# Kernel tuning notes

Measured on AMD Instinct MI355X. Metric: run time of the kernel, lower is better.

Reference implementation:

```python
import jax, jax.numpy as jnp
import numpy as np

D_IN = 1024
D_OUT = 1024
NUM_HEAD = 16
HEAD_DIM = D_OUT // NUM_HEAD


def setup_inputs() -> dict:
    key = jax.random.key(0)
    ks = jax.random.split(key, 7)
    B, S = 2, 2048
    X = jax.random.normal(ks[0], (B, S, D_IN), dtype=jnp.float32)
    scale = 1.0 / np.sqrt(D_IN)
    Wq = jax.random.normal(ks[1], (D_IN, D_OUT), dtype=jnp.float32) * scale
    Wk = jax.random.normal(ks[2], (D_IN, D_OUT), dtype=jnp.float32) * scale
    Wv = jax.random.normal(ks[3], (D_IN, D_OUT), dtype=jnp.float32) * scale
    bq = jax.random.normal(ks[4], (D_OUT,), dtype=jnp.float32) * 0.01
    bk = jax.random.normal(ks[5], (D_OUT,), dtype=jnp.float32) * 0.01
    bv = jax.random.normal(ks[6], (D_OUT,), dtype=jnp.float32) * 0.01
    return {"X": X, "Wq": Wq, "bq": bq, "Wk": Wk, "bk": bk, "Wv": Wv, "bv": bv}


def reference(X, Wq, bq, Wk, bk, Wv, bv):
    B, S, _ = X.shape
    # QKV projections, reshape to [B, H, S, Dh]
    def proj(W, b):
        y = jnp.einsum('bsi,io->bso', X, W) + b
        return y.reshape(B, S, NUM_HEAD, HEAD_DIM).transpose(0, 2, 1, 3)
    Q = proj(Wq, bq)
    K = proj(Wk, bk)
    V = proj(Wv, bv)
    # NOTE: original divides by head_dim**2 (not sqrt(head_dim)) -- kept faithful.
    scores = jnp.einsum('bhqd,bhkd->bhqk', Q, K) / (HEAD_DIM ** 2)
    attn = jax.nn.softmax(scores, axis=-1)  # dropout is identity at eval
    out = jnp.einsum('bhqk,bhkd->bhqd', attn, V)
    return out.transpose(0, 2, 1, 3).reshape(B, S, D_OUT)
```

## Files before the change

### kernel.cpp

```cpp
#include <hip/hip_runtime.h>
#include <hip/hip_bf16.h>

typedef __attribute__((ext_vector_type(8))) short frag8;
typedef __attribute__((ext_vector_type(8))) unsigned short u16x8;
typedef __attribute__((ext_vector_type(4))) float f32x4;

__device__ __forceinline__ unsigned short f2b(float x) {
    unsigned int u = __float_as_uint(x);
    return (unsigned short)((u + 0x7FFFu + ((u >> 16) & 1u)) >> 16);
}

__device__ __forceinline__ int swz(int row, int scol) {
    return (row << 6) + (scol ^ ((row & 7) << 3));
}

__global__ __launch_bounds__(256) void xcvt_kernel(const float* __restrict__ X,
                                                   unsigned short* __restrict__ Xb)
{
    const int i = (blockIdx.x * 256 + threadIdx.x) * 8;
    float4 a = *reinterpret_cast<const float4*>(X + i);
    float4 b = *reinterpret_cast<const float4*>(X + i + 4);
    u16x8 v;
    v[0] = f2b(a.x); v[1] = f2b(a.y); v[2] = f2b(a.z); v[3] = f2b(a.w);
    v[4] = f2b(b.x); v[5] = f2b(b.y); v[6] = f2b(b.z); v[7] = f2b(b.w);
    *reinterpret_cast<u16x8*>(Xb + i) = v;
}

__global__ __launch_bounds__(256) void transpose_w_kernel(
    const float* __restrict__ Wq, const float* __restrict__ Wk, const float* __restrict__ Wv,
    unsigned short* __restrict__ Wtq, unsigned short* __restrict__ Wtk, unsigned short* __restrict__ Wtv)
{
    const float* W = blockIdx.z == 0 ? Wq : (blockIdx.z == 1 ? Wk : Wv);
    unsigned short* Wt = blockIdx.z == 0 ? Wtq : (blockIdx.z == 1 ? Wtk : Wtv);
    __shared__ unsigned short tile[64 * 72];
    const int t = threadIdx.x;
    const int k0 = blockIdx.x * 64, n0 = blockIdx.y * 64;
#pragma unroll
    for (int r = 0; r < 16; ++r) {
        int k = r * 4 + (t >> 6), n = t & 63;
        tile[n * 72 + k] = f2b(W[(size_t)(k0 + k) * 1024 + n0 + n]);
    }
    __syncthreads();
#pragma unroll
    for (int r = 0; r < 16; ++r) {
        int n = r * 4 + (t >> 6), k = t & 63;
        Wt[(size_t)(n0 + n) * 1024 + k0 + k] = tile[n * 72 + k];
    }
}

__global__ __launch_bounds__(256, 3) void proj_kernel(
    const unsigned short* __restrict__ Xb,
    const unsigned short* __restrict__ Wtq, const unsigned short* __restrict__ Wtk,
    const unsigned short* __restrict__ Wtv,
    const float* __restrict__ bq, const float* __restrict__ bk, const float* __restrict__ bv,
    unsigned short* __restrict__ Qw, unsigned short* __restrict__ Kw, unsigned short* __restrict__ Vw)
{
    const unsigned short* Wt = blockIdx.z == 0 ? Wtq : (blockIdx.z == 1 ? Wtk : Wtv);
    const float* bias        = blockIdx.z == 0 ? bq  : (blockIdx.z == 1 ? bk  : bv);
    unsigned short* Out      = blockIdx.z == 0 ? Qw  : (blockIdx.z == 1 ? Kw  : Vw);

    __shared__ unsigned short As[128 * 64];
    __shared__ unsigned short Bs[128 * 64];

    const int t = threadIdx.x, lane = t & 63, w = t >> 6;
    const int wr = w >> 1, wc = w & 1;
    const int l15 = lane & 15, lhi = lane >> 4;
    const int row0 = blockIdx.x * 128, n0 = blockIdx.y * 128;

    const int sr = t >> 3;
    const int ss = (t & 7) * 8;
    const unsigned short* Ag = Xb + (size_t)(row0 + sr) * 1024 + ss;
    const unsigned short* Bg = Wt + (size_t)(n0 + sr) * 1024 + ss;

    float4 ar0 = *reinterpret_cast<const float4*>(Ag);
    float4 ar1 = *reinterpret_cast<const float4*>(Ag + 32 * 1024);
    float4 ar2 = *reinterpret_cast<const float4*>(Ag + 64 * 1024);
    float4 ar3 = *reinterpret_cast<const float4*>(Ag + 96 * 1024);
    float4 br0 = *reinterpret_cast<const float4*>(Bg);
    float4 br1 = *reinterpret_cast<const float4*>(Bg + 32 * 1024);
    float4 br2 = *reinterpret_cast<const float4*>(Bg + 64 * 1024);
    float4 br3 = *reinterpret_cast<const float4*>(Bg + 96 * 1024);

    f32x4 acc[4][4];
#pragma unroll
    for (int i = 0; i < 4; ++i)
#pragma unroll
        for (int j = 0; j < 4; ++j) acc[i][j] = (f32x4){0.f, 0.f, 0.f, 0.f};

    for (int k0 = 0; k0 < 1024; k0 += 64) {
        *reinterpret_cast<float4*>(&As[swz(sr,      ss)]) = ar0;
        *reinterpret_cast<float4*>(&As[swz(sr + 32, ss)]) = ar1;
        *reinterpret_cast<float4*>(&As[swz(sr + 64, ss)]) = ar2;
        *reinterpret_cast<float4*>(&As[swz(sr + 96, ss)]) = ar3;
        *reinterpret_cast<float4*>(&Bs[swz(sr,      ss)]) = br0;
        *reinterpret_cast<float4*>(&Bs[swz(sr + 32, ss)]) = br1;
        *reinterpret_cast<float4*>(&Bs[swz(sr + 64, ss)]) = br2;
        *reinterpret_cast<float4*>(&Bs[swz(sr + 96, ss)]) = br3;
        __syncthreads();
        if (k0 < 960) {
            const unsigned short* An = Ag + k0 + 64;
            const unsigned short* Bn = Bg + k0 + 64;
            ar0 = *reinterpret_cast<const float4*>(An);
            ar1 = *reinterpret_cast<const float4*>(An + 32 * 1024);
            ar2 = *reinterpret_cast<const float4*>(An + 64 * 1024);
            ar3 = *reinterpret_cast<const float4*>(An + 96 * 1024);
            br0 = *reinterpret_cast<const float4*>(Bn);
            br1 = *reinterpret_cast<const float4*>(Bn + 32 * 1024);
            br2 = *reinterpret_cast<const float4*>(Bn + 64 * 1024);
            br3 = *reinterpret_cast<const float4*>(Bn + 96 * 1024);
        }
#pragma unroll
        for (int kk = 0; kk < 2; ++kk) {
            frag8 af[4], bf[4];
#pragma unroll
            for (int i = 0; i < 4; ++i)
                af[i] = *reinterpret_cast<const frag8*>(&As[swz(wr * 64 + i * 16 + l15, kk * 32 + lhi * 8)]);
#pragma unroll
            for (int j = 0; j < 4; ++j)
                bf[j] = *reinterpret_cast<const frag8*>(&Bs[swz(wc * 64 + j * 16 + l15, kk * 32 + lhi * 8)]);
#pragma unroll
            for (int i = 0; i < 4; ++i)
#pragma unroll
                for (int j = 0; j < 4; ++j)
                    acc[i][j] = __builtin_amdgcn_mfma_f32_16x16x32_bf16(af[i], bf[j], acc[i][j], 0, 0, 0);
        }
        __syncthreads();
    }

    if (blockIdx.z != 2) {
#pragma unroll
        for (int j = 0; j < 4; ++j) {
            int cc = n0 + wc * 64 + j * 16 + l15;
            float bsv = bias[cc];
            int hh = cc >> 6, dd = cc & 63;
#pragma unroll
            for (int i = 0; i < 4; ++i) {
#pragma unroll
                for (int e = 0; e < 4; ++e) {
                    int rr = row0 + wr * 64 + i * 16 + lhi * 4 + e;
                    int bb = rr >> 11, ss2 = rr & 2047;
                    Out[((size_t)(bb * 16 + hh) * 2048 + ss2) * 64 + dd] = f2b(acc[i][j][e] + bsv);
                }
            }
        }
    } else {
#pragma unroll
        for (int j = 0; j < 4; ++j) {
            int cc = n0 + wc * 64 + j * 16 + l15;
            float bsv = bias[cc];
            int hh = cc >> 6, dd = cc & 63;
#pragma unroll
            for (int i = 0; i < 4; ++i) {
                int rr = row0 + wr * 64 + i * 16 + lhi * 4;
                int bb = rr >> 11, ss2 = rr & 2047;
                ushort4 us;
                us.x = f2b(acc[i][j][0] + bsv);
                us.y = f2b(acc[i][j][1] + bsv);
                us.z = f2b(acc[i][j][2] + bsv);
                us.w = f2b(acc[i][j][3] + bsv);
                *reinterpret_cast<ushort4*>(&Out[((size_t)(bb * 16 + hh) * 64 + dd) * 2048 + ss2]) = us;
            }
        }
    }
}

__global__ __launch_bounds__(512, 4) void attn_kernel(
    const unsigned short* __restrict__ Qw, const unsigned short* __restrict__ Kw,
    const unsigned short* __restrict__ VT, float* __restrict__ out)
{
    __shared__ unsigned short Ks[2][64 * 64];
    __shared__ unsigned short Vt[2][64 * 64];
    __shared__ unsigned short Pl[128 * 64];

    const int t = threadIdx.x, lane = t & 63, w = t >> 6;
    const int hwid = blockIdx.x + 16 * blockIdx.y;
    const int lid  = (hwid & 7) * 64 + (hwid >> 3);
    const int lx = lid & 15, bh = lid >> 4;
    const size_t base = (size_t)bh * (2048 * 64);
    const int q0 = lx * 128;
    const int l15 = lane & 15, lhi = lane >> 4;

    frag8 qf0, qf1;
    {
        int row = t >> 2;
        int s0 = (t & 3) * 16;
        const float4* qp = reinterpret_cast<const float4*>(Qw + base + (size_t)(q0 + row) * 64 + s0);
        float4 a = qp[0], b = qp[1];
        *reinterpret_cast<float4*>(&Pl[swz(row, s0)]) = a;
        *reinterpret_cast<float4*>(&Pl[swz(row, s0 + 8)]) = b;
        int qrow = w * 16 + l15;
        qf0 = *reinterpret_cast<const frag8*>(&Pl[swz(qrow, lhi * 8)]);
        qf1 = *reinterpret_cast<const frag8*>(&Pl[swz(qrow, 32 + lhi * 8)]);
    }

    const int sr = t >> 3;
    const int ss = (t & 7) * 8;

    float4 kreg = *reinterpret_cast<const float4*>(Kw + base + (size_t)sr * 64 + ss);
    float4 vreg = *reinterpret_cast<const float4*>(VT + base + (size_t)sr * 2048 + ss);

    f32x4 acc_o[4];
#pragma unroll
    for (int j = 0; j < 4; ++j) acc_o[j] = (f32x4){0.f, 0.f, 0.f, 0.f};
    f32x4 acc_den = (f32x4){0.f, 0.f, 0.f, 0.f};

    frag8 ones;
#pragma unroll
    for (int e = 0; e < 8; ++e) ones[e] = (short)0x3F80;

    const float sc = 1.0f / 4096.0f;
    const int prow = w * 16 + l15;

    int buf = 0;
    for (int kt = 0; kt < 32; ++kt) {
        *reinterpret_cast<float4*>(&Ks[buf][swz(sr, ss)]) = kreg;
        *reinterpret_cast<float4*>(&Vt[buf][swz(sr, ss)]) = vreg;
        __syncthreads();
        if (kt < 31) {
            int k0n = (kt + 1) * 64;
            kreg = *reinterpret_cast<const float4*>(Kw + base + (size_t)(k0n + sr) * 64 + ss);
            vreg = *reinterpret_cast<const float4*>(VT + base + (size_t)sr * 2048 + k0n + ss);
        }

        f32x4 accs[4];
#pragma unroll
        for (int j = 0; j < 4; ++j) accs[j] = (f32x4){0.f, 0.f, 0.f, 0.f};
#pragma unroll
        for (int j = 0; j < 4; ++j) {
            frag8 kf = *reinterpret_cast<const frag8*>(&Ks[buf][swz(j * 16 + l15, lhi * 8)]);
            accs[j] = __builtin_amdgcn_mfma_f32_16x16x32_bf16(kf, qf0, accs[j], 0, 0, 0);
        }
#pragma unroll
        for (int j = 0; j < 4; ++j) {
            frag8 kf = *reinterpret_cast<const frag8*>(&Ks[buf][swz(j * 16 + l15, 32 + lhi * 8)]);
            accs[j] = __builtin_amdgcn_mfma_f32_16x16x32_bf16(kf, qf1, accs[j], 0, 0, 0);
        }

#pragma unroll
        for (int j = 0; j < 4; ++j) {
            unsigned int u0 = __float_as_uint(__expf(accs[j][0] * sc));
            unsigned int u1 = __float_as_uint(__expf(accs[j][1] * sc));
            unsigned int u2 = __float_as_uint(__expf(accs[j][2] * sc));
            unsigned int u3 = __float_as_uint(__expf(accs[j][3] * sc));
            unsigned int lo = ((u0 + 0x8000u) >> 16) | ((u1 + 0x8000u) & 0xFFFF0000u);
            unsigned int hi = ((u2 + 0x8000u) >> 16) | ((u3 + 0x8000u) & 0xFFFF0000u);
            *reinterpret_cast<uint2*>(&Pl[swz(prow, j * 16 + lhi * 4)]) = make_uint2(lo, hi);
        }

#pragma unroll
        for (int ks = 0; ks < 2; ++ks) {
            frag8 pf = *reinterpret_cast<const frag8*>(&Pl[swz(prow, ks * 32 + lhi * 8)]);
            acc_den = __builtin_amdgcn_mfma_f32_16x16x32_bf16(pf, ones, acc_den, 0, 0, 0);
#pragma unroll
            for (int j = 0; j < 4; ++j) {
                frag8 vf = *reinterpret_cast<const frag8*>(&Vt[buf][swz(j * 16 + l15, ks * 32 + lhi * 8)]);
                acc_o[j] = __builtin_amdgcn_mfma_f32_16x16x32_bf16(pf, vf, acc_o[j], 0, 0, 0);
            }
        }
        buf ^= 1;
    }

    const int b = bh >> 4, h = bh & 15;
#pragma unroll
    for (int j = 0; j < 4; ++j) {
#pragma unroll
        for (int i = 0; i < 4; ++i) {
            int q = q0 + w * 16 + lhi * 4 + i;
            out[((size_t)b * 2048 + q) * 1024 + h * 64 + j * 16 + l15] = acc_o[j][i] / acc_den[i];
        }
    }
}

extern "C" void kernel_launch(void* const* d_in, const int* in_sizes, int n_in,
                              void* d_out, int out_size, void* d_ws, size_t ws_size,
                              hipStream_t stream) {
    const float* X  = (const float*)d_in[0];
    const float* Wq = (const float*)d_in[1];
    const float* bq = (const float*)d_in[2];
    const float* Wk = (const float*)d_in[3];
    const float* bk = (const float*)d_in[4];
    const float* Wv = (const float*)d_in[5];
    const float* bv = (const float*)d_in[6];

    unsigned short* ws  = (unsigned short*)d_ws;
    unsigned short* Wtq = ws;
    unsigned short* Wtk = Wtq + 1048576;
    unsigned short* Wtv = Wtk + 1048576;
    unsigned short* Xb  = Wtv + 1048576;
    unsigned short* Qw  = Xb + 4194304;
    unsigned short* Kw  = Qw + 4194304;
    unsigned short* Vw  = Kw + 4194304;
    float* out = (float*)d_out;

    xcvt_kernel<<<dim3(2048), 256, 0, stream>>>(X, Xb);
    transpose_w_kernel<<<dim3(16, 16, 3), 256, 0, stream>>>(Wq, Wk, Wv, Wtq, Wtk, Wtv);
    proj_kernel<<<dim3(32, 8, 3), 256, 0, stream>>>(Xb, Wtq, Wtk, Wtv, bq, bk, bv, Qw, Kw, Vw);
    attn_kernel<<<dim3(16, 32), 512, 0, stream>>>(Qw, Kw, Vw, out);
}
```

Baseline: 97.23 us.

## Keep softmax P in registers by permuting K rows, drop P LDS buffer

```diff
diff --git a/kernel.cpp b/kernel.cpp
--- a/kernel.cpp
+++ b/kernel.cpp
@@ -170,7 +170,6 @@
 {
     __shared__ unsigned short Ks[2][64 * 64];
     __shared__ unsigned short Vt[2][64 * 64];
-    __shared__ unsigned short Pl[128 * 64];
 
     const int t = threadIdx.x, lane = t & 63, w = t >> 6;
     const int hwid = blockIdx.x + 16 * blockIdx.y;
@@ -180,24 +179,28 @@
     const int q0 = lx * 128;
     const int l15 = lane & 15, lhi = lane >> 4;
 
+    const int sr = t >> 3;
+    const int ss = (t & 7) * 8;
+    const int srho = (sr & 51) | ((sr & 4) << 1) | ((sr & 8) >> 1);
+
+    float4 kreg = *reinterpret_cast<const float4*>(Kw + base + (size_t)sr * 64 + ss);
+    float4 vreg = *reinterpret_cast<const float4*>(VT + base + (size_t)sr * 2048 + ss);
+
     frag8 qf0, qf1;
     {
+        unsigned short* Qs = &Vt[0][0];
         int row = t >> 2;
         int s0 = (t & 3) * 16;
         const float4* qp = reinterpret_cast<const float4*>(Qw + base + (size_t)(q0 + row) * 64 + s0);
         float4 a = qp[0], b = qp[1];
-        *reinterpret_cast<float4*>(&Pl[swz(row, s0)]) = a;
-        *reinterpret_cast<float4*>(&Pl[swz(row, s0 + 8)]) = b;
+        *reinterpret_cast<float4*>(&Qs[swz(row, s0)]) = a;
+        *reinterpret_cast<float4*>(&Qs[swz(row, s0 + 8)]) = b;
+        __syncthreads();
         int qrow = w * 16 + l15;
-        qf0 = *reinterpret_cast<const frag8*>(&Pl[swz(qrow, lhi * 8)]);
-        qf1 = *reinterpret_cast<const frag8*>(&Pl[swz(qrow, 32 + lhi * 8)]);
-    }
-
-    const int sr = t >> 3;
-    const int ss = (t & 7) * 8;
-
-    float4 kreg = *reinterpret_cast<const float4*>(Kw + base + (size_t)sr * 64 + ss);
-    float4 vreg = *reinterpret_cast<const float4*>(VT + base + (size_t)sr * 2048 + ss);
+        qf0 = *reinterpret_cast<const frag8*>(&Qs[swz(qrow, lhi * 8)]);
+        qf1 = *reinterpret_cast<const frag8*>(&Qs[swz(qrow, 32 + lhi * 8)]);
+        __syncthreads();
+    }
 
     f32x4 acc_o[4];
 #pragma unroll
@@ -209,11 +212,11 @@
     for (int e = 0; e < 8; ++e) ones[e] = (short)0x3F80;
 
     const float sc = 1.0f / 4096.0f;
-    const int prow = w * 16 + l15;
+    const int krbase = ((l15 >> 3) & 1) * 16 + ((l15 >> 2) & 1) * 4 + (l15 & 3);
 
     int buf = 0;
     for (int kt = 0; kt < 32; ++kt) {
-        *reinterpret_cast<float4*>(&Ks[buf][swz(sr, ss)]) = kreg;
+        *reinterpret_cast<float4*>(&Ks[buf][swz(srho, ss)]) = kreg;
         *reinterpret_cast<float4*>(&Vt[buf][swz(sr, ss)]) = vreg;
         __syncthreads();
         if (kt < 31) {
@@ -224,39 +227,45 @@
 
         f32x4 accs[4];
 #pragma unroll
-        for (int j = 0; j < 4; ++j) accs[j] = (f32x4){0.f, 0.f, 0.f, 0.f};
-#pragma unroll
-        for (int j = 0; j < 4; ++j) {
-            frag8 kf = *reinterpret_cast<const frag8*>(&Ks[buf][swz(j * 16 + l15, lhi * 8)]);
-            accs[j] = __builtin_amdgcn_mfma_f32_16x16x32_bf16(kf, qf0, accs[j], 0, 0, 0);
-        }
-#pragma unroll
-        for (int j = 0; j < 4; ++j) {
-            frag8 kf = *reinterpret_cast<const frag8*>(&Ks[buf][swz(j * 16 + l15, 32 + lhi * 8)]);
-            accs[j] = __builtin_amdgcn_mfma_f32_16x16x32_bf16(kf, qf1, accs[j], 0, 0, 0);
-        }
-
-#pragma unroll
-        for (int j = 0; j < 4; ++j) {
-            unsigned int u0 = __float_as_uint(__expf(accs[j][0] * sc));
-            unsigned int u1 = __float_as_uint(__expf(accs[j][1] * sc));
-            unsigned int u2 = __float_as_uint(__expf(accs[j][2] * sc));
-            unsigned int u3 = __float_as_uint(__expf(accs[j][3] * sc));
-            unsigned int lo = ((u0 + 0x8000u) >> 16) | ((u1 + 0x8000u) & 0xFFFF0000u);
-            unsigned int hi = ((u2 + 0x8000u) >> 16) | ((u3 + 0x8000u) & 0xFFFF0000u);
-            *reinterpret_cast<uint2*>(&Pl[swz(prow, j * 16 + lhi * 4)]) = make_uint2(lo, hi);
-        }
-
+        for (int m = 0; m < 4; ++m) accs[m] = (f32x4){0.f, 0.f, 0.f, 0.f};
+        __builtin_amdgcn_s_setprio(1);
+#pragma unroll
+        for (int m = 0; m < 4; ++m) {
+            int krow = krbase + (m >> 1) * 32 + (m & 1) * 8;
+            frag8 kfa = *reinterpret_cast<const frag8*>(&Ks[buf][swz(krow, lhi * 8)]);
+            accs[m] = __builtin_amdgcn_mfma_f32_16x16x32_bf16(kfa, qf0, accs[m], 0, 0, 0);
+            frag8 kfb = *reinterpret_cast<const frag8*>(&Ks[buf][swz(krow, 32 + lhi * 8)]);
+            accs[m] = __builtin_amdgcn_mfma_f32_16x16x32_bf16(kfb, qf1, accs[m], 0, 0, 0);
+        }
+        __builtin_amdgcn_s_setprio(0);
+
+        unsigned int pk[8];
+#pragma unroll
+        for (int m = 0; m < 4; ++m) {
+            unsigned int u0 = __float_as_uint(__expf(accs[m][0] * sc));
+            unsigned int u1 = __float_as_uint(__expf(accs[m][1] * sc));
+            unsigned int u2 = __float_as_uint(__expf(accs[m][2] * sc));
+            unsigned int u3 = __float_as_uint(__expf(accs[m][3] * sc));
+            pk[2 * m]     = ((u0 + 0x8000u) >> 16) | ((u1 + 0x8000u) & 0xFFFF0000u);
+            pk[2 * m + 1] = ((u2 + 0x8000u) >> 16) | ((u3 + 0x8000u) & 0xFFFF0000u);
+        }
+
+        __builtin_amdgcn_s_setprio(1);
 #pragma unroll
         for (int ks = 0; ks < 2; ++ks) {
-            frag8 pf = *reinterpret_cast<const frag8*>(&Pl[swz(prow, ks * 32 + lhi * 8)]);
-            acc_den = __builtin_amdgcn_mfma_f32_16x16x32_bf16(pf, ones, acc_den, 0, 0, 0);
+            union { frag8 f; unsigned int u[4]; } pa;
+            pa.u[0] = pk[4 * ks];
+            pa.u[1] = pk[4 * ks + 1];
+            pa.u[2] = pk[4 * ks + 2];
+            pa.u[3] = pk[4 * ks + 3];
+            acc_den = __builtin_amdgcn_mfma_f32_16x16x32_bf16(pa.f, ones, acc_den, 0, 0, 0);
 #pragma unroll
             for (int j = 0; j < 4; ++j) {
                 frag8 vf = *reinterpret_cast<const frag8*>(&Vt[buf][swz(j * 16 + l15, ks * 32 + lhi * 8)]);
-                acc_o[j] = __builtin_amdgcn_mfma_f32_16x16x32_bf16(pf, vf, acc_o[j], 0, 0, 0);
+                acc_o[j] = __builtin_amdgcn_mfma_f32_16x16x32_bf16(pa.f, vf, acc_o[j], 0, 0, 0);
             }
         }
+        __builtin_amdgcn_s_setprio(0);
         buf ^= 1;
     }
 
```

Result: faster. 92.58 us (-4.8%).
